# Kernel optimization log

Hardware: AMD Instinct MI355X
Metric: run time of the kernel (lower is better)

The kernel has to match this reference:

```python
import jax, jax.numpy as jnp
import numpy as np

B, T, C, H = 8, 2048, 1024, 64

def setup_inputs() -> dict:
    key = jax.random.key(0)
    ks = jax.random.split(key, 8)
    s = 1.0 / np.sqrt(C)  # ~Linear init scale
    return {
        "x_real": jax.random.normal(ks[0], (B, T, C), jnp.float32),
        "x_imag": jax.random.normal(ks[1], (B, T, C), jnp.float32),
        "Wk_r": jax.random.normal(ks[2], (C, H), jnp.float32) * s,
        "Wk_i": jax.random.normal(ks[3], (C, H), jnp.float32) * s,
        "Wq_r": jax.random.normal(ks[4], (C, H), jnp.float32) * s,
        "Wq_i": jax.random.normal(ks[5], (C, H), jnp.float32) * s,
        "Wv_r": jax.random.normal(ks[6], (C, H), jnp.float32) * s,
        "Wv_i": jax.random.normal(ks[7], (C, H), jnp.float32) * s,
    }

def _complex_linear(x_real, x_imag, Wr, Wi):
    # (xr + i xi) @ (Wr + i Wi)
    out_real = x_real @ Wr - x_imag @ Wi
    out_imag = x_imag @ Wr + x_real @ Wi
    return out_real, out_imag

def reference(x_real, x_imag, Wk_r, Wk_i, Wq_r, Wq_i, Wv_r, Wv_i):
    k_r, k_i = _complex_linear(x_real, x_imag, Wk_r, Wk_i)
    q_r, q_i = _complex_linear(x_real, x_imag, Wq_r, Wq_i)
    v_r, v_i = _complex_linear(x_real, x_imag, Wv_r, Wv_i)
    # complex scores: q @ conj(k)^T equivalent per source math
    wei_real = jnp.einsum('bqh,bkh->bqk', q_r, k_r) + jnp.einsum('bqh,bkh->bqk', q_i, k_i)
    wei_imag = jnp.einsum('bqh,bkh->bqk', q_i, k_r) - jnp.einsum('bqh,bkh->bqk', q_r, k_i)
    eps = 1e-4
    wei_mag = jnp.sqrt(wei_real**2 + wei_imag**2 + eps) * (H ** -0.5)
    causal = jnp.tril(jnp.ones((T, T), dtype=bool))
    wei_mag = jnp.where(causal, wei_mag, -jnp.inf)
    wei = jax.nn.softmax(wei_mag, axis=-1)  # dropout p=0.0 -> identity
    out_real = jnp.einsum('bqk,bkh->bqh', wei, v_r)
    out_imag = jnp.einsum('bqk,bkh->bqh', wei, v_i)
    return out_real, out_imag
```

## Files before the change

### kernel.cpp

```cpp
#include <hip/hip_runtime.h>
#include <hip/hip_bf16.h>
#include <math.h>

#define BB 8
#define TT 2048
#define CC 1024
#define HH 64
#define NROW (BB*TT)
#define NST (NROW*HH)
#define KK2 2048
#define NN 384
#define GN 256
#define VTP 2080

typedef __attribute__((ext_vector_type(8))) short short8;
typedef __attribute__((ext_vector_type(4))) float f32x4;

static __device__ inline unsigned pk_bf16(float a, float b) {
    __hip_bfloat162 h = __float22bfloat162_rn(make_float2(a, b));
    unsigned u; __builtin_memcpy(&u, &h, 4); return u;
}
static __device__ inline short f2bf_s(float a) {
    __hip_bfloat16 h = __float2bfloat16(a);
    short s; __builtin_memcpy(&s, &h, 2); return s;
}
static __device__ inline short8 neg8(short8 a) {
    short8 r;
    #pragma unroll
    for (int i = 0; i < 8; ++i) r[i] = a[i] ^ (short)0x8000;
    return r;
}

static __device__ inline void async16(const void* g, void* l) {
    __builtin_amdgcn_global_load_lds(
        (const __attribute__((address_space(1))) void*)g,
        (__attribute__((address_space(3))) void*)l,
        16, 0, 0);
}

__global__ __launch_bounds__(256) void prep_kernel(
    const float* __restrict__ Wkr, const float* __restrict__ Wki,
    const float* __restrict__ Wqr, const float* __restrict__ Wqi,
    const float* __restrict__ Wvr, const float* __restrict__ Wvi,
    short* __restrict__ Bt)
{
    const int n = blockIdx.x;
    const int g = n >> 6, h = n & 63;
    const int p = g >> 1;
    const bool im = g & 1;
    const float* Wr = (p == 0) ? Wkr : (p == 1) ? Wqr : Wvr;
    const float* Wi = (p == 0) ? Wki : (p == 1) ? Wqi : Wvi;
    const float* W1 = im ? Wi : Wr;
    const float* W2 = im ? Wr : Wi;
    const float s2 = im ? 1.f : -1.f;

    #pragma unroll
    for (int j = 0; j < 8; ++j) {
        int k = threadIdx.x + 256 * j;
        float v = (k < CC) ? W1[k * HH + h] : s2 * W2[(k - CC) * HH + h];
        Bt[(size_t)n * KK2 + k] = f2bf_s(v);
    }
}

#define LDP 72
#define STP 136

__global__ __launch_bounds__(256) void proj_gemm(
    const float* __restrict__ xr, const float* __restrict__ xi,
    const short* __restrict__ Bt,
    short* __restrict__ G, short* __restrict__ VT)
{
    __shared__ __attribute__((aligned(16))) float sAf[128 * 64];
    __shared__ __attribute__((aligned(16))) short sB[64 * 64];

    const int tid = threadIdx.x;
    const int mbase = blockIdx.x * 128;
    const int comp = blockIdx.y;

    const int wave = tid >> 6, lane = tid & 63;
    const int quad = lane >> 4, lm = lane & 15;

    const int lgrp = lane >> 3;
    const int lslot = lane & 7;
    const int scolB = ((lslot ^ lgrp) << 4);

    const int arow_l = lane >> 4;
    const int acol_l = lane & 15;

    const char* Bg = (const char*)(Bt + (size_t)comp * 64 * KK2);

    f32x4 acc[2][4] = {};

    for (int ks = 0; ks < KK2 / 64; ++ks) {
        const float* __restrict__ srcA = (ks < 16) ? xr : xi;
        const int kc = (ks & 15) * 64;

        #pragma unroll
        for (int i = 0; i < 8; ++i) {
            int q = wave * 8 + i;
            int r = q * 4 + arow_l;
            int c = acol_l ^ (r & 7);
            async16((const char*)(srcA + (size_t)(mbase + r) * CC + kc) + (c << 4),
                    (char*)sAf + q * 1024);
        }
        #pragma unroll
        for (int i = 0; i < 2; ++i) {
            int q = wave * 2 + i;
            async16(Bg + (size_t)(q * 8 + lgrp) * (KK2 * 2) + ks * 128 + scolB,
                    (char*)sB + q * 1024);
        }
        __syncthreads();

        #pragma unroll
        for (int kk = 0; kk < 2; ++kk) {
            short8 af[2];
            #pragma unroll
            for (int mi = 0; mi < 2; ++mi) {
                const int row = 32 * wave + 16 * mi + lm;
                const int c0 = 8 * kk + 2 * quad;
                const int s = row & 7;
                f32x4 a0 = *(const f32x4*)&sAf[row * 64 + ((c0 ^ s) << 2)];
                f32x4 a1 = *(const f32x4*)&sAf[row * 64 + (((c0 + 1) ^ s) << 2)];
                uint4 u;
                u.x = pk_bf16(a0[0], a0[1]);
                u.y = pk_bf16(a0[2], a0[3]);
                u.z = pk_bf16(a1[0], a1[1]);
                u.w = pk_bf16(a1[2], a1[3]);
                __builtin_memcpy(&af[mi], &u, 16);
            }
            const int cs = (kk * 32 + quad * 8) ^ ((lm & 7) << 3);
            short8 bf[4];
            #pragma unroll
            for (int ni = 0; ni < 4; ++ni)
                bf[ni] = *(const short8*)&sB[(16 * ni + lm) * 64 + cs];

            #pragma unroll
            for (int mi = 0; mi < 2; ++mi)
                #pragma unroll
                for (int ni = 0; ni < 4; ++ni)
                    acc[mi][ni] = __builtin_amdgcn_mfma_f32_16x16x32_bf16(
                        af[mi], bf[ni], acc[mi][ni], 0, 0, 0);
        }
        __syncthreads();
    }

    if (comp < 4) {
        short* sG = (short*)sAf;
        #pragma unroll
        for (int mi = 0; mi < 2; ++mi)
            #pragma unroll
            for (int ni = 0; ni < 4; ++ni)
                #pragma unroll
                for (int r = 0; r < 4; ++r)
                    sG[(32*wave + 16*mi + quad*4 + r) * LDP + 16*ni + lm] =
                        f2bf_s(acc[mi][ni][r]);
        __syncthreads();
        #pragma unroll
        for (int j = 0; j < 4; ++j) {
            int id = tid + 256 * j;
            int row = id >> 3, c8 = id & 7;
            uint4 v = *(const uint4*)&sG[row * LDP + c8 * 8];
            *(uint4*)&G[(size_t)(mbase + row) * GN + comp*64 + c8*8] = v;
        }
    } else {
        short* sT = (short*)sAf;
        const int vcomp = comp - 4;
        const int b = mbase >> 11;
        const int tb = mbase & 2047;
        #pragma unroll
        for (int mi = 0; mi < 2; ++mi)
            #pragma unroll
            for (int ni = 0; ni < 4; ++ni)
                #pragma unroll
                for (int r = 0; r < 4; ++r)
                    sT[(16*ni + lm) * STP + 32*wave + 16*mi + quad*4 + r] =
                        f2bf_s(acc[mi][ni][r]);
        __syncthreads();
        #pragma unroll
        for (int j = 0; j < 4; ++j) {
            int id = tid + 256 * j;
            int h = id >> 4, c = id & 15;
            uint4 v = *(const uint4*)&sT[h * STP + c * 8];
            *(uint4*)&VT[(((size_t)vcomp*BB + b)*64 + h)*VTP + tb + c*8] = v;
        }
    }
}

#define PLDS 72
#define SC2 0.18033688f

__global__ __launch_bounds__(256) void attn_kernel(
    const short* __restrict__ G,
    const short* __restrict__ VT,
    float* __restrict__ out)
{
    __shared__ float comb[4][16][128];
    __shared__ float cmw[4][16], clw[4][16];

    const int tid = threadIdx.x;
    const int wave = tid >> 6, lane = tid & 63;
    const int quad = lane >> 4, lm = lane & 15;
    const int b = blockIdx.x;
    const int j = (int)(gridDim.y - 1) - (int)blockIdx.y;
    const int qbase = j * 16;
    const int nkt = (j >> 2) + 1;

    const short* Qrow = G + ((size_t)(b*TT + qbase + lm)) * GN + 128;
    short8 A1[4], A2[4];
    #pragma unroll
    for (int ks = 0; ks < 4; ++ks)
        A1[ks] = *(const short8*)(Qrow + ks*32 + quad*8);
    A2[0] = A1[2]; A2[1] = A1[3];
    A2[2] = neg8(A1[0]); A2[3] = neg8(A1[1]);

    short8 ones;
    #pragma unroll
    for (int i = 0; i < 8; ++i) ones[i] = (short)0x3F80;

    f32x4 Or[4], Oi[4];
    #pragma unroll
    for (int h = 0; h < 4; ++h)
        #pragma unroll
        for (int r = 0; r < 4; ++r) { Or[h][r] = 0.f; Oi[h][r] = 0.f; }
    f32x4 Ol = {0.f, 0.f, 0.f, 0.f};
    float m[4];
    #pragma unroll
    for (int r = 0; r < 4; ++r) m[r] = -INFINITY;

    short* Pw = (short*)&comb[wave][0][0];
    const short* Vrb = VT + (size_t)b * 64 * VTP;
    const short* Vib = VT + ((size_t)BB + b) * 64 * VTP;

    for (int kt = wave; kt < nkt; kt += 4) {
        const int kb = kt * 64;
        const short* Kt = G + ((size_t)(b*TT + kb)) * GN;

        short8 Kf[4][4];
        #pragma unroll
        for (int nt = 0; nt < 4; ++nt) {
            const short* Krow = Kt + (size_t)(nt*16 + lm) * GN;
            #pragma unroll
            for (int ks = 0; ks < 4; ++ks)
                Kf[nt][ks] = *(const short8*)(Krow + ks*32 + quad*8);
        }

        f32x4 mag[4];
        #pragma unroll
        for (int nt = 0; nt < 4; ++nt) {
            f32x4 sr = {0.f,0.f,0.f,0.f}, si = {0.f,0.f,0.f,0.f};
            __builtin_amdgcn_s_setprio(1);
            #pragma unroll
            for (int ks = 0; ks < 4; ++ks) {
                sr = __builtin_amdgcn_mfma_f32_16x16x32_bf16(A1[ks], Kf[nt][ks], sr, 0,0,0);
                si = __builtin_amdgcn_mfma_f32_16x16x32_bf16(A2[ks], Kf[nt][ks], si, 0,0,0);
            }
            __builtin_amdgcn_s_setprio(0);
            int tok = kb + nt*16 + lm;
            #pragma unroll
            for (int r = 0; r < 4; ++r) {
                float v = __builtin_amdgcn_sqrtf(
                              fmaf(sr[r], sr[r], fmaf(si[r], si[r], 1e-4f))) * SC2;
                int qrow = qbase + quad*4 + r;
                mag[nt][r] = (tok > qrow) ? -INFINITY : v;
            }
        }

        short8 Vr[4][2], Vi[4][2];
        #pragma unroll
        for (int ht = 0; ht < 4; ++ht) {
            const short* vr0 = Vrb + (size_t)(ht*16 + lm) * VTP + kb + quad*8;
            const short* vi0 = Vib + (size_t)(ht*16 + lm) * VTP + kb + quad*8;
            Vr[ht][0] = *(const short8*)(vr0);
            Vr[ht][1] = *(const short8*)(vr0 + 32);
            Vi[ht][0] = *(const short8*)(vi0);
            Vi[ht][1] = *(const short8*)(vi0 + 32);
        }

        float tm[4];
        #pragma unroll
        for (int r = 0; r < 4; ++r)
            tm[r] = fmaxf(fmaxf(mag[0][r], mag[1][r]), fmaxf(mag[2][r], mag[3][r]));
        #pragma unroll
        for (int d = 1; d < 16; d <<= 1)
            #pragma unroll
            for (int r = 0; r < 4; ++r)
                tm[r] = fmaxf(tm[r], __shfl_xor(tm[r], d, 16));

        int need = (tm[0] > m[0] + 8.f) | (tm[1] > m[1] + 8.f) |
                   (tm[2] > m[2] + 8.f) | (tm[3] > m[3] + 8.f);
        if (__any(need)) {
            float al[4];
            #pragma unroll
            for (int r = 0; r < 4; ++r) {
                float mn = fmaxf(m[r], tm[r]);
                al[r] = __builtin_amdgcn_exp2f(m[r] - mn);
                m[r] = mn;
            }
            #pragma unroll
            for (int h = 0; h < 4; ++h)
                #pragma unroll
                for (int r = 0; r < 4; ++r) { Or[h][r] *= al[r]; Oi[h][r] *= al[r]; }
            #pragma unroll
            for (int r = 0; r < 4; ++r) Ol[r] *= al[r];
        }

        #pragma unroll
        for (int nt = 0; nt < 4; ++nt)
            #pragma unroll
            for (int r = 0; r < 4; ++r) {
                float p = __builtin_amdgcn_exp2f(mag[nt][r] - m[r]);
                Pw[(quad*4 + r) * PLDS + nt*16 + lm] = f2bf_s(p);
            }
        short8 Af0 = *(const short8*)&Pw[lm * PLDS + quad*8];
        short8 Af1 = *(const short8*)&Pw[lm * PLDS + 32 + quad*8];

        __builtin_amdgcn_s_setprio(1);
        Ol = __builtin_amdgcn_mfma_f32_16x16x32_bf16(Af0, ones, Ol, 0,0,0);
        Ol = __builtin_amdgcn_mfma_f32_16x16x32_bf16(Af1, ones, Ol, 0,0,0);
        __builtin_amdgcn_s_setprio(0);

        #pragma unroll
        for (int ht = 0; ht < 4; ++ht) {
            __builtin_amdgcn_s_setprio(1);
            Or[ht] = __builtin_amdgcn_mfma_f32_16x16x32_bf16(Af0, Vr[ht][0], Or[ht], 0,0,0);
            Or[ht] = __builtin_amdgcn_mfma_f32_16x16x32_bf16(Af1, Vr[ht][1], Or[ht], 0,0,0);
            Oi[ht] = __builtin_amdgcn_mfma_f32_16x16x32_bf16(Af0, Vi[ht][0], Oi[ht], 0,0,0);
            Oi[ht] = __builtin_amdgcn_mfma_f32_16x16x32_bf16(Af1, Vi[ht][1], Oi[ht], 0,0,0);
            __builtin_amdgcn_s_setprio(0);
        }
    }

    __syncthreads();

    #pragma unroll
    for (int ht = 0; ht < 4; ++ht)
        #pragma unroll
        for (int r = 0; r < 4; ++r) {
            comb[wave][quad*4 + r][ht*16 + lm]      = Or[ht][r];
            comb[wave][quad*4 + r][64 + ht*16 + lm] = Oi[ht][r];
        }
    if (lm == 0) {
        #pragma unroll
        for (int r = 0; r < 4; ++r) {
            cmw[wave][quad*4 + r] = m[r];
            clw[wave][quad*4 + r] = Ol[r];
        }
    }
    __syncthreads();

    for (int e = tid; e < 16*128; e += 256) {
        int q = e >> 7, h = e & 127;
        float mstar = fmaxf(fmaxf(cmw[0][q], cmw[1][q]), fmaxf(cmw[2][q], cmw[3][q]));
        float osum = 0.f, lsum = 0.f;
        #pragma unroll
        for (int w = 0; w < 4; ++w) {
            float f = __builtin_amdgcn_exp2f(cmw[w][q] - mstar);
            osum = fmaf(f, comb[w][q][h], osum);
            lsum = fmaf(f, clw[w][q], lsum);
        }
        float res = osum / lsum;
        int comp = h >> 6, hh = h & 63;
        out[(size_t)comp * NST + ((size_t)(b*TT + qbase + q)) * HH + hh] = res;
    }
}

extern "C" void kernel_launch(void* const* d_in, const int* in_sizes, int n_in,
                              void* d_out, int out_size, void* d_ws, size_t ws_size,
                              hipStream_t stream)
{
    const float* xr  = (const float*)d_in[0];
    const float* xi  = (const float*)d_in[1];
    const float* Wkr = (const float*)d_in[2];
    const float* Wki = (const float*)d_in[3];
    const float* Wqr = (const float*)d_in[4];
    const float* Wqi = (const float*)d_in[5];
    const float* Wvr = (const float*)d_in[6];
    const float* Wvi = (const float*)d_in[7];

    short* Bt = (short*)d_ws;
    short* G  = (short*)((char*)d_ws + (2u  << 20));
    short* VT = (short*)((char*)d_ws + (11u << 20));
    float* out = (float*)d_out;

    prep_kernel<<<NN, 256, 0, stream>>>(Wkr, Wki, Wqr, Wqi, Wvr, Wvi, Bt);

    dim3 g1(NROW / 128, 6);
    proj_gemm<<<g1, 256, 0, stream>>>(xr, xi, Bt, G, VT);

    dim3 g3(BB, TT / 16);
    attn_kernel<<<g3, 256, 0, stream>>>(G, VT, out);
}
```

Measured before the change: 246.3 us.

## Double-buffer projection GEMM shared-memory tiles with async prefetch of next K-phase

Splits the projection GEMM's K loop into 32-wide phases and keeps two shared-memory buffers, so async global-to-LDS loads for phase ph+2 are in flight while phase ph is computed. It uses explicit vmcnt waits and raw barriers in place of __syncthreads, and redoes the swizzle for the narrower tiles. This is meant to hide global load latency in the projection stage, at the cost of more barriers per K step and hand-tuned wait counts that must match the number of outstanding loads.

```diff
diff --git a/kernel.cpp b/kernel.cpp
--- a/kernel.cpp
+++ b/kernel.cpp
@@ -64,14 +64,16 @@
 
 #define LDP 72
 #define STP 136
+#define APH (128*32)
+#define BPH (64*32)
 
 __global__ __launch_bounds__(256) void proj_gemm(
     const float* __restrict__ xr, const float* __restrict__ xi,
     const short* __restrict__ Bt,
     short* __restrict__ G, short* __restrict__ VT)
 {
-    __shared__ __attribute__((aligned(16))) float sAf[128 * 64];
-    __shared__ __attribute__((aligned(16))) short sB[64 * 64];
+    __shared__ __attribute__((aligned(16))) float sA[2 * APH];
+    __shared__ __attribute__((aligned(16))) short sB[2 * BPH];
 
     const int tid = threadIdx.x;
     const int mbase = blockIdx.x * 128;
@@ -80,72 +82,95 @@
     const int wave = tid >> 6, lane = tid & 63;
     const int quad = lane >> 4, lm = lane & 15;
 
-    const int lgrp = lane >> 3;
-    const int lslot = lane & 7;
-    const int scolB = ((lslot ^ lgrp) << 4);
-
-    const int arow_l = lane >> 4;
-    const int acol_l = lane & 15;
+    const int arow = lane >> 3;
+    const int asrc = (lane & 7) ^ arow;
+    const int brow = lane >> 2;
+    const int bsrc = (lane & 3) ^ ((lane >> 3) & 3);
 
     const char* Bg = (const char*)(Bt + (size_t)comp * 64 * KK2);
 
     f32x4 acc[2][4] = {};
 
-    for (int ks = 0; ks < KK2 / 64; ++ks) {
-        const float* __restrict__ srcA = (ks < 16) ? xr : xi;
-        const int kc = (ks & 15) * 64;
-
-        #pragma unroll
-        for (int i = 0; i < 8; ++i) {
-            int q = wave * 8 + i;
-            int r = q * 4 + arow_l;
-            int c = acol_l ^ (r & 7);
-            async16((const char*)(srcA + (size_t)(mbase + r) * CC + kc) + (c << 4),
-                    (char*)sAf + q * 1024);
-        }
-        #pragma unroll
-        for (int i = 0; i < 2; ++i) {
-            int q = wave * 2 + i;
-            async16(Bg + (size_t)(q * 8 + lgrp) * (KK2 * 2) + ks * 128 + scolB,
-                    (char*)sB + q * 1024);
-        }
-        __syncthreads();
-
-        #pragma unroll
-        for (int kk = 0; kk < 2; ++kk) {
-            short8 af[2];
-            #pragma unroll
-            for (int mi = 0; mi < 2; ++mi) {
-                const int row = 32 * wave + 16 * mi + lm;
-                const int c0 = 8 * kk + 2 * quad;
-                const int s = row & 7;
-                f32x4 a0 = *(const f32x4*)&sAf[row * 64 + ((c0 ^ s) << 2)];
-                f32x4 a1 = *(const f32x4*)&sAf[row * 64 + (((c0 + 1) ^ s) << 2)];
-                uint4 u;
-                u.x = pk_bf16(a0[0], a0[1]);
-                u.y = pk_bf16(a0[2], a0[3]);
-                u.z = pk_bf16(a1[0], a1[1]);
-                u.w = pk_bf16(a1[2], a1[3]);
-                __builtin_memcpy(&af[mi], &u, 16);
-            }
-            const int cs = (kk * 32 + quad * 8) ^ ((lm & 7) << 3);
-            short8 bf[4];
-            #pragma unroll
-            for (int ni = 0; ni < 4; ++ni)
-                bf[ni] = *(const short8*)&sB[(16 * ni + lm) * 64 + cs];
-
-            #pragma unroll
-            for (int mi = 0; mi < 2; ++mi)
-                #pragma unroll
-                for (int ni = 0; ni < 4; ++ni)
-                    acc[mi][ni] = __builtin_amdgcn_mfma_f32_16x16x32_bf16(
-                        af[mi], bf[ni], acc[mi][ni], 0, 0, 0);
-        }
-        __syncthreads();
-    }
+    #define STAGE_PH(ph, BUF) do {                                              \
+        const int ks_ = (ph) >> 1;                                              \
+        const float* __restrict__ sa_ = (ks_ < 16) ? xr : xi;                   \
+        const int kc_ = (ks_ & 15) * 64 + ((ph) & 1) * 32;                      \
+        _Pragma("unroll")                                                       \
+        for (int i_ = 0; i_ < 4; ++i_) {                                        \
+            int q_ = wave * 4 + i_;                                             \
+            int r_ = q_ * 8 + arow;                                             \
+            async16((const char*)(sa_ + (size_t)(mbase + r_) * CC + kc_)        \
+                        + (asrc << 4),                                          \
+                    (char*)(sA + (BUF) * APH) + q_ * 1024);                     \
+        }                                                                       \
+        async16(Bg + (size_t)(wave * 16 + brow) * (KK2 * 2)                     \
+                    + ks_ * 128 + ((ph) & 1) * 64 + (bsrc << 4),                \
+                (char*)(sB + (BUF) * BPH) + wave * 1024);                       \
+    } while (0)
+
+    #define COMPUTE_PH(BUF) do {                                                \
+        const float* sAp_ = sA + (BUF) * APH;                                   \
+        const short* sBp_ = sB + (BUF) * BPH;                                   \
+        short8 af_[2];                                                          \
+        _Pragma("unroll")                                                       \
+        for (int mi_ = 0; mi_ < 2; ++mi_) {                                     \
+            const int row_ = 32 * wave + 16 * mi_ + lm;                         \
+            const int s_ = lm & 7;                                              \
+            f32x4 a0_ = *(const f32x4*)&sAp_[row_ * 32 + (((2*quad)   ^ s_) << 2)]; \
+            f32x4 a1_ = *(const f32x4*)&sAp_[row_ * 32 + (((2*quad+1) ^ s_) << 2)]; \
+            uint4 u_;                                                           \
+            u_.x = pk_bf16(a0_[0], a0_[1]);                                     \
+            u_.y = pk_bf16(a0_[2], a0_[3]);                                     \
+            u_.z = pk_bf16(a1_[0], a1_[1]);                                     \
+            u_.w = pk_bf16(a1_[2], a1_[3]);                                     \
+            __builtin_memcpy(&af_[mi_], &u_, 16);                               \
+        }                                                                       \
+        short8 bf_[4];                                                          \
+        _Pragma("unroll")                                                       \
+        for (int ni_ = 0; ni_ < 4; ++ni_)                                       \
+            bf_[ni_] = *(const short8*)&sBp_[(16 * ni_ + lm) * 32               \
+                        + ((quad ^ ((lm >> 1) & 3)) << 3)];                     \
+        _Pragma("unroll")                                                       \
+        for (int mi_ = 0; mi_ < 2; ++mi_)                                       \
+            _Pragma("unroll")                                                   \
+            for (int ni_ = 0; ni_ < 4; ++ni_)                                   \
+                acc[mi_][ni_] = __builtin_amdgcn_mfma_f32_16x16x32_bf16(        \
+                    af_[mi_], bf_[ni_], acc[mi_][ni_], 0, 0, 0);                \
+    } while (0)
+
+    STAGE_PH(0, 0);
+    STAGE_PH(1, 1);
+
+    for (int ph = 0; ph < 62; ph += 2) {
+        asm volatile("s_waitcnt vmcnt(5)" ::: "memory");
+        __builtin_amdgcn_s_barrier();
+        __builtin_amdgcn_sched_barrier(0);
+        COMPUTE_PH(0);
+        __builtin_amdgcn_sched_barrier(0);
+        __builtin_amdgcn_s_barrier();
+        STAGE_PH(ph + 2, 0);
+
+        asm volatile("s_waitcnt vmcnt(5)" ::: "memory");
+        __builtin_amdgcn_s_barrier();
+        __builtin_amdgcn_sched_barrier(0);
+        COMPUTE_PH(1);
+        __builtin_amdgcn_sched_barrier(0);
+        __builtin_amdgcn_s_barrier();
+        STAGE_PH(ph + 3, 1);
+    }
+    asm volatile("s_waitcnt vmcnt(5)" ::: "memory");
+    __builtin_amdgcn_s_barrier();
+    __builtin_amdgcn_sched_barrier(0);
+    COMPUTE_PH(0);
+    asm volatile("s_waitcnt vmcnt(0)" ::: "memory");
+    __builtin_amdgcn_s_barrier();
+    __builtin_amdgcn_sched_barrier(0);
+    COMPUTE_PH(1);
+
+    __syncthreads();
 
     if (comp < 4) {
-        short* sG = (short*)sAf;
+        short* sG = (short*)sA;
         #pragma unroll
         for (int mi = 0; mi < 2; ++mi)
             #pragma unroll
@@ -163,7 +188,7 @@
             *(uint4*)&G[(size_t)(mbase + row) * GN + comp*64 + c8*8] = v;
         }
     } else {
-        short* sT = (short*)sAf;
+        short* sT = (short*)sA;
         const int vcomp = comp - 4;
         const int b = mbase >> 11;
         const int tb = mbase & 2047;
@@ -184,6 +209,8 @@
             *(uint4*)&VT[(((size_t)vcomp*BB + b)*64 + h)*VTP + tb + c*8] = v;
         }
     }
+    #undef STAGE_PH
+    #undef COMPUTE_PH
 }
 
 #define PLDS 72
```

Measured after the change: 261.8 us. 1.06x slower.
